# Performance work log

Measured on AMD Instinct MI355X. Metric: run time of the kernel, lower is better.

Reference implementation:

```python
import jax, jax.numpy as jnp
from jax import lax
import numpy as np

B, H, W, C = 8, 32, 32, 256
SOFTMAX_SCALE = 10.0
DN = ('NHWC', 'HWIO', 'NHWC')


def _patches(t):
    # t: [b,h,w,c] -> [b,h,w,3,3,c], SAME zero padding, stride 1 (tf.image.extract_patches)
    b, h, w, c = t.shape
    tp = jnp.pad(t, ((0, 0), (1, 1), (1, 1), (0, 0)))
    cols = [tp[:, i:i + h, j:j + w, :] for i in range(3) for j in range(3)]
    return jnp.stack(cols, axis=3).reshape(b, h, w, 3, 3, c)


def _diag_fuse(z):
    # conv2d of [L,L] map with eye(3) kernel, SAME padding:
    # out[i,j] = z[i-1,j-1] + z[i,j] + z[i+1,j+1] (zero padded)
    dr = jnp.pad(z, ((1, 0), (1, 0)))[:-1, :-1]
    ul = jnp.pad(z, ((0, 1), (0, 1)))[1:, 1:]
    return z + dr + ul


def _conv(x, w):
    return lax.conv_general_dilated(x, w, (1, 1), 'SAME', dimension_numbers=DN)


def _attend(xi, wi, mmean):
    # xi: [h,w,c]; wi: [3,3,c,L] patch kernels; mmean: [L] mean of mask patches
    h, w, c = xi.shape
    L = h * w
    norm = jnp.maximum(jnp.sqrt(jnp.sum(wi * wi, axis=(0, 1, 2))), 1e-4)
    yi = _conv(xi[None], wi / norm)[0]  # [h,w,L] cosine-sim scores
    # fuse: diagonal propagation along both spatial orderings
    z = yi.reshape(L, L)
    z = _diag_fuse(z).reshape(h, w, h, w).transpose(1, 0, 3, 2).reshape(L, L)
    z = _diag_fuse(z).reshape(w, h, w, h).transpose(1, 0, 3, 2)  # [h,w,h,w]
    yi = z.reshape(h, w, L)
    mm = (mmean == 1.0).astype(yi.dtype)  # valid-patch mask per location
    yi = jax.nn.softmax(yi * mm * SOFTMAX_SCALE, axis=-1) * mm
    # conv2d_transpose(yi, wi, stride 1, SAME) == conv with hw-flipped kernel,
    # in/out channels swapped (TF filter layout [h,w,out=C,in=L])
    k2 = jnp.flip(wi, (0, 1)).transpose(0, 1, 3, 2)  # [3,3,L,C]
    return _conv(yi[None], k2)[0]  # [h,w,c]


def _forward(x, mask, conv_w, conv_b, conv1_w, conv1_b, conv2_w, conv2_b):
    b, h, w, c = x.shape
    L = h * w
    # rate=1: tf.image.resize to same size is identity, f == b == x
    wi = _patches(x).reshape(b, L, 3, 3, c).transpose(0, 2, 3, 4, 1)  # [b,3,3,c,L]
    mmean = _patches(mask).mean(axis=(3, 4, 5)).reshape(b, L)
    y = jax.vmap(_attend)(x, wi, mmean)  # [b,h,w,c]
    ycat = jnp.concatenate([y, x], axis=-1)  # [b,h,w,2c]
    g1 = jax.nn.sigmoid(_conv(ycat, conv1_w) + conv1_b)
    g2 = jax.nn.sigmoid(_conv(ycat, conv2_w) + conv2_b)
    gate = (g1 + g2) * 0.5
    out = gate * (_conv(ycat, conv_w) + conv_b)
    return out, jnp.ones_like(mask)


def setup_inputs() -> dict:
    key = jax.random.key(0)
    ks = jax.random.split(key, 4)
    x = jax.random.normal(ks[0], (B, H, W, C), jnp.float32)
    mask = jnp.ones((B, H, W, 1), jnp.float32)
    conv_w = jax.random.normal(ks[1], (3, 3, 2 * C, C), jnp.float32) * 0.02
    conv_b = jnp.zeros((C,), jnp.float32)
    conv1_w = jax.random.normal(ks[2], (1, 1, 2 * C, C), jnp.float32) * 0.02
    conv1_b = jnp.zeros((C,), jnp.float32)
    conv2_w = jax.random.normal(ks[3], (3, 3, 2 * C, C), jnp.float32) * 0.02
    conv2_b = jnp.zeros((C,), jnp.float32)
    return {'x': x, 'mask': mask, 'conv_w': conv_w, 'conv_b': conv_b,
            'conv1_w': conv1_w, 'conv1_b': conv1_b, 'conv2_w': conv2_w, 'conv2_b': conv2_b}


def reference(x, mask, conv_w, conv_b, conv1_w, conv1_b, conv2_w, conv2_b):
    return _forward(x, mask, conv_w, conv_b, conv1_w, conv1_b, conv2_w, conv2_b)
```

## Files before the change

### kernel.cpp

```cpp
#include <hip/hip_runtime.h>
#include <math.h>

typedef unsigned short u16;
typedef __bf16 bf16x8 __attribute__((ext_vector_type(8)));
typedef float f32x4 __attribute__((ext_vector_type(4)));

#define NPOS 1156
#define GSTR 1160
#define GOFF (GSTR * 1156)
#define YSTR 1032
#define YOFF (YSTR * 1026)
#define POS34(p) ((((p) >> 5) + 1) * 34 + ((p) & 31) + 1)

__device__ __constant__ const int kDiagOff[9] = {
    -35 * (GSTR + 1), -34 * (GSTR + 1), -33 * (GSTR + 1),
    -1 * (GSTR + 1),  0,                1 * (GSTR + 1),
    33 * (GSTR + 1),  34 * (GSTR + 1),  35 * (GSTR + 1)};

__device__ __forceinline__ u16 f2bf(float f) {
  unsigned int u = __builtin_bit_cast(unsigned int, f);
  return (u16)((u + 0x7FFFu + ((u >> 16) & 1u)) >> 16);
}
__device__ __forceinline__ float bf2f(u16 v) {
  unsigned int u = ((unsigned int)v) << 16;
  return __builtin_bit_cast(float, u);
}
__device__ __forceinline__ void gload16(const void* g, void* l) {
  __builtin_amdgcn_global_load_lds(
      (const __attribute__((address_space(1))) void*)g,
      (__attribute__((address_space(3))) void*)l, 16, 0, 0);
}
__device__ __forceinline__ int posOf(int p) { return POS34(p); }

__global__ __launch_bounds__(256) void zb_pre(
    float* __restrict__ Gpad, u16* __restrict__ Ylin,
    u16* __restrict__ xpad, u16* __restrict__ ypad) {
  int bi = blockIdx.x, tid = threadIdx.x;
  if (bi < 9248) {
    int b = bi / 1156, r = bi - b * 1156;
    float* row = Gpad + (size_t)b * GOFF + (size_t)r * GSTR;
    int rm = r % 34;
    bool brow = (r < 34) || (r >= 1122) || (rm == 0) || (rm == 33);
    if (brow) {
      for (int c = tid; c < GSTR; c += 256) row[c] = 0.f;
    } else {
      for (int c = tid; c < GSTR; c += 256) {
        int cm = c % 34;
        if (c < 34 || c >= 1122 || cm == 0 || cm == 33) row[c] = 0.f;
      }
    }
    return;
  }
  bi -= 9248;
  if (bi < 8208) {
    int b = bi / 1026, r = bi - b * 1026;
    u16* row = Ylin + (size_t)b * YOFF + (size_t)r * YSTR;
    if (r == 0 || r == 1025) {
      for (int c = tid; c < YSTR; c += 256) row[c] = 0;
    } else if (tid < 8) {
      row[tid == 0 ? 0 : 1024 + tid] = 0;
    }
    return;
  }
  bi -= 8208;
  int arr = bi / 9248;
  bi -= arr * 9248;
  int b = bi / 1156, p = bi - b * 1156;
  int pm = p % 34;
  bool bp = (p < 34) || (p >= 1122) || (pm == 0) || (pm == 33);
  if (!bp) return;
  u16* dst = (arr ? ypad : xpad) + ((size_t)b * NPOS + p) * 256;
  dst[tid] = 0;
}

__global__ __launch_bounds__(256) void zb_apad(u16* __restrict__ Apad2) {
  int bi = blockIdx.x, tid = threadIdx.x;
  int b = bi / 1156, r = bi - b * 1156;
  u16* row = Apad2 + (size_t)b * GOFF + (size_t)r * GSTR;
  int rm = r % 34;
  bool brow = (r < 34) || (r >= 1122) || (rm == 0) || (rm == 33);
  if (brow) {
    for (int c = tid; c < GSTR; c += 256) row[c] = 0;
  } else {
    for (int c = tid; c < GSTR; c += 256) {
      int cm = c % 34;
      if (c < 34 || c >= 1122 || cm == 0 || cm == 33) row[c] = 0;
    }
  }
}

__global__ __launch_bounds__(256) void cast_x(
    const float* __restrict__ x, u16* __restrict__ xpad, u16* __restrict__ xT) {
  int blk = blockIdx.x;
  int b = blk >> 5, h = blk & 31;
  __shared__ u16 T[256][33];
  const float* xrow = x + ((size_t)b * 1024 + h * 32) * 256;
  int tid = threadIdx.x;
  for (int idx = tid; idx < 8192; idx += 256) {
    int w = idx >> 8, c = idx & 255;
    u16 v = f2bf(xrow[(size_t)w * 256 + c]);
    T[c][w] = v;
    xpad[((size_t)b * NPOS + (h + 1) * 34 + (w + 1)) * 256 + c] = v;
  }
  __syncthreads();
  int c = tid;
  unsigned int* dp = (unsigned int*)(xT + ((size_t)(b * 256 + c)) * 1024 + h * 32);
  const unsigned int* sp = (const unsigned int*)&T[c][0];
#pragma unroll
  for (int u = 0; u < 16; ++u) dp[u] = sp[u];
}

__global__ __launch_bounds__(256) void wtrans(
    const float* __restrict__ src, u16* __restrict__ dst, int K) {
  int k0 = blockIdx.x * 32;
  __shared__ u16 T[256][34];
  int tid = threadIdx.x;
  for (int idx = tid; idx < 8192; idx += 256) {
    int kr = idx >> 8, c = idx & 255;
    T[c][kr] = f2bf(src[(size_t)(k0 + kr) * 256 + c]);
  }
  __syncthreads();
  int c = tid;
  unsigned int* dp = (unsigned int*)(dst + (size_t)c * K + k0);
  const unsigned int* sp = (const unsigned int*)&T[c][0];
#pragma unroll
  for (int u = 0; u < 16; ++u) dp[u] = sp[u];
}

__global__ __launch_bounds__(256) void gram_base(
    const u16* __restrict__ xpad, float* __restrict__ Gpad) {
  const int b = blockIdx.z;
  const int m0 = blockIdx.x << 7;
  const int n0 = blockIdx.y << 7;
  const u16* xb = xpad + (size_t)b * NPOS * 256;
  __shared__ __align__(16) u16 As[128 * 64];
  __shared__ __align__(16) u16 Bs[128 * 64];
  const int tid = threadIdx.x;
  const int lane = tid & 63;
  const int wave = tid >> 6;
  const int wm = wave >> 1, wn = wave & 1;
  const int srow = lane >> 3;
  const int cswz = ((lane & 7) ^ srow) << 3;
  int pa[4], pb[4];
#pragma unroll
  for (int i = 0; i < 4; ++i) {
    pa[i] = posOf(m0 + wave * 32 + i * 8 + srow);
    pb[i] = posOf(n0 + wave * 32 + i * 8 + srow);
  }
  int aidx[4][2], bidx[4][2];
#pragma unroll
  for (int f = 0; f < 4; ++f)
#pragma unroll
    for (int ks = 0; ks < 2; ++ks) {
      int ra = wm * 64 + f * 16 + (lane & 15);
      int rb = wn * 64 + f * 16 + (lane & 15);
      int k16 = ks * 4 + (lane >> 4);
      aidx[f][ks] = ra * 64 + ((k16 ^ (ra & 7)) << 3);
      bidx[f][ks] = rb * 64 + ((k16 ^ (rb & 7)) << 3);
    }
  f32x4 acc[4][4] = {};
  for (int c0 = 0; c0 < 256; c0 += 64) {
    __syncthreads();
#pragma unroll
    for (int i = 0; i < 4; ++i) {
      gload16(xb + (size_t)pa[i] * 256 + c0 + cswz, &As[(wave * 32 + i * 8) * 64]);
      gload16(xb + (size_t)pb[i] * 256 + c0 + cswz, &Bs[(wave * 32 + i * 8) * 64]);
    }
    __syncthreads();
#pragma unroll
    for (int ks = 0; ks < 2; ++ks) {
      bf16x8 a[4], bb[4];
#pragma unroll
      for (int f = 0; f < 4; ++f) a[f] = *(const bf16x8*)(As + aidx[f][ks]);
#pragma unroll
      for (int f = 0; f < 4; ++f) bb[f] = *(const bf16x8*)(Bs + bidx[f][ks]);
#pragma unroll
      for (int mi = 0; mi < 4; ++mi)
#pragma unroll
        for (int ni = 0; ni < 4; ++ni)
          acc[mi][ni] = __builtin_amdgcn_mfma_f32_16x16x32_bf16(a[mi], bb[ni], acc[mi][ni], 0, 0, 0);
    }
  }
  float* Gb = Gpad + (size_t)b * GOFF;
  const int r0 = (lane >> 4) << 2;
  const int cb0 = n0 + wn * 64 + (lane & 15);
#pragma unroll
  for (int mi = 0; mi < 4; ++mi) {
    int row = m0 + wm * 64 + mi * 16 + r0;
    int rp = POS34(row);
#pragma unroll
    for (int ni = 0; ni < 4; ++ni) {
      int cp = POS34(cb0 + ni * 16);
#pragma unroll
      for (int r = 0; r < 4; ++r)
        Gb[(size_t)(rp + r) * GSTR + cp] = acc[mi][ni][r];
    }
  }
}

__global__ __launch_bounds__(256) void norm_mm(
    const float* __restrict__ Gpad, const float* __restrict__ mask,
    float* __restrict__ invn, float* __restrict__ mm, float* __restrict__ ones_out) {
  int idx = blockIdx.x * 256 + threadIdx.x;
  int b = idx >> 10, l = idx & 1023;
  const float* Gb = Gpad + (size_t)b * GOFF;
  size_t dbase = (size_t)POS34(l) * (GSTR + 1);
  float d = 0.f;
#pragma unroll
  for (int t = 0; t < 9; ++t) d += Gb[dbase + kDiagOff[t]];
  invn[idx] = 1.0f / fmaxf(sqrtf(d), 1e-4f);
  int lh = l >> 5, lw = l & 31;
  float s = 0.f;
  for (int dh = -1; dh <= 1; ++dh)
    for (int dw = -1; dw <= 1; ++dw) {
      int hh = lh + dh, wv = lw + dw;
      if (hh >= 0 && hh < 32 && wv >= 0 && wv < 32) s += mask[b * 1024 + hh * 32 + wv];
    }
  mm[idx] = ((s / 9.0f) == 1.0f) ? 1.0f : 0.0f;
  ones_out[idx] = 1.0f;
}

__global__ __launch_bounds__(256) void patch_norm_p(
    const float* __restrict__ Gpad, const float* __restrict__ invn,
    u16* __restrict__ Ylin) {
  const int b = blockIdx.y;
  const int p0 = blockIdx.x << 2;
  const float* Gb = Gpad + (size_t)b * GOFF;
  u16* Yb = Ylin + (size_t)b * YOFF;
  const int tid = threadIdx.x;
  const int l0 = tid << 2;
  const int lp0 = POS34(l0);
  const float4 iv = *(const float4*)(invn + (b << 10) + l0);
#pragma unroll
  for (int r = 0; r < 4; ++r) {
    int p = p0 + r;
    int base = POS34(p) * GSTR + lp0;
    float v[9][4];
#pragma unroll
    for (int t = 0; t < 9; ++t) {
      const float* q = Gb + (base + kDiagOff[t]);
      v[t][0] = q[0]; v[t][1] = q[1]; v[t][2] = q[2]; v[t][3] = q[3];
    }
    float s0 = 0.f, s1 = 0.f, s2 = 0.f, s3 = 0.f;
#pragma unroll
    for (int t = 0; t < 9; ++t) { s0 += v[t][0]; s1 += v[t][1]; s2 += v[t][2]; s3 += v[t][3]; }
    u16* yw = Yb + (size_t)(p + 1) * YSTR + l0 + 1;
    yw[0] = f2bf(s0 * iv.x); yw[1] = f2bf(s1 * iv.y);
    yw[2] = f2bf(s2 * iv.z); yw[3] = f2bf(s3 * iv.w);
  }
}

__device__ __forceinline__ float z1p(const u16* __restrict__ Yb, int r, int c) {
  size_t a = (size_t)(r + 1) * YSTR + (c + 1);
  return bf2f(Yb[a]) + bf2f(Yb[a - (YSTR + 1)]) + bf2f(Yb[a + (YSTR + 1)]);
}

__global__ __launch_bounds__(256) void fuse_softmax(
    const u16* __restrict__ Ylin, const float* __restrict__ mm,
    u16* __restrict__ Apad2) {
  const int bi = blockIdx.x;
  const int b = bi >> 10, i = bi & 1023;
  const u16* Yb = Ylin + (size_t)b * YOFF;
  __shared__ float smm[1024];
  __shared__ float red[256];
  const int tid = threadIdx.x;
  for (int t = tid; t < 1024; t += 256) smm[t] = mm[(b << 10) + t];
  __syncthreads();
  const int si = ((i & 31) << 5) | (i >> 5);
  const int rm = (si >= 1) ? ((((si - 1) & 31) << 5) | ((si - 1) >> 5)) : -1;
  const int rp = (si <= 1022) ? ((((si + 1) & 31) << 5) | ((si + 1) >> 5)) : -1;
  float logit[4];
  float lmax = -3.0e38f;
#pragma unroll
  for (int q = 0; q < 4; ++q) {
    int j = tid + (q << 8);
    int sj = ((j & 31) << 5) | (j >> 5);
    float S = z1p(Yb, i, j);
    if (rm >= 0 && sj >= 1) {
      int col = (((sj - 1) & 31) << 5) | ((sj - 1) >> 5);
      S += z1p(Yb, rm, col);
    }
    if (rp >= 0 && sj <= 1022) {
      int col = (((sj + 1) & 31) << 5) | ((sj + 1) >> 5);
      S += z1p(Yb, rp, col);
    }
    float lg = S * smm[j] * 10.0f;
    logit[q] = lg;
    lmax = fmaxf(lmax, lg);
  }
  red[tid] = lmax; __syncthreads();
  for (int off = 128; off > 0; off >>= 1) {
    if (tid < off) red[tid] = fmaxf(red[tid], red[tid + off]);
    __syncthreads();
  }
  float M = red[0];
  __syncthreads();
  float ex[4];
  float lsum = 0.f;
#pragma unroll
  for (int q = 0; q < 4; ++q) { ex[q] = expf(logit[q] - M); lsum += ex[q]; }
  red[tid] = lsum; __syncthreads();
  for (int off = 128; off > 0; off >>= 1) {
    if (tid < off) red[tid] += red[tid + off];
    __syncthreads();
  }
  float inv = 1.0f / red[0];
  u16* Ap = Apad2 + (size_t)b * GOFF + (size_t)POS34(i) * GSTR;
#pragma unroll
  for (int q = 0; q < 4; ++q) {
    int j = tid + (q << 8);
    Ap[POS34(j)] = f2bf(smm[j] * ex[q] * inv);
  }
}

__global__ __launch_bounds__(256) void afuse_p(
    const u16* __restrict__ Apad2, u16* __restrict__ Afuse) {
  const int b = blockIdx.y;
  const int q0 = blockIdx.x << 2;
  const u16* Ab = Apad2 + (size_t)b * GOFF;
  u16* Fb = Afuse + ((size_t)b << 20);
  const int tid = threadIdx.x;
  const int l0 = tid << 2;
  const int lp0 = POS34(l0);
#pragma unroll
  for (int r = 0; r < 4; ++r) {
    int q = q0 + r;
    int base = POS34(q) * GSTR + lp0;
    float v[9][4];
#pragma unroll
    for (int t = 0; t < 9; ++t) {
      const u16* p = Ab + (base - kDiagOff[t]);
      v[t][0] = bf2f(p[0]); v[t][1] = bf2f(p[1]);
      v[t][2] = bf2f(p[2]); v[t][3] = bf2f(p[3]);
    }
    float s0 = 0.f, s1 = 0.f, s2 = 0.f, s3 = 0.f;
#pragma unroll
    for (int t = 0; t < 9; ++t) { s0 += v[t][0]; s1 += v[t][1]; s2 += v[t][2]; s3 += v[t][3]; }
    u16* fw = Fb + (size_t)q * 1024 + l0;
    fw[0] = f2bf(s0); fw[1] = f2bf(s1); fw[2] = f2bf(s2); fw[3] = f2bf(s3);
  }
}

__global__ __launch_bounds__(256) void paste_gemm(
    const u16* __restrict__ Afuse, const u16* __restrict__ xT, u16* __restrict__ ypad) {
  const int bm0 = blockIdx.x << 6;
  const int b = bm0 >> 10;
  const int q0 = bm0 & 1023;
  const int n0 = blockIdx.y << 6;
  const u16* Ab = Afuse + ((size_t)b << 20);
  const u16* xTb = xT + ((size_t)b << 18);
  __shared__ __align__(16) u16 As[64 * 64];
  __shared__ __align__(16) u16 Bs[64 * 64];
  const int tid = threadIdx.x;
  const int lane = tid & 63;
  const int wave = tid >> 6;
  const int wm = wave >> 1, wn = wave & 1;
  const int srow = lane >> 3;
  const int cswz = ((lane & 7) ^ srow) << 3;
  int aidx[2][2], bidx[2][2];
#pragma unroll
  for (int ks = 0; ks < 2; ++ks) {
    int k16 = ks * 4 + (lane >> 4);
#pragma unroll
    for (int f = 0; f < 2; ++f) {
      int ra = wm * 32 + f * 16 + (lane & 15);
      aidx[f][ks] = ra * 64 + ((k16 ^ (ra & 7)) << 3);
      int rb = wn * 32 + f * 16 + (lane & 15);
      bidx[f][ks] = rb * 64 + ((k16 ^ (rb & 7)) << 3);
    }
  }
  f32x4 acc[2][2] = {};
  for (int l0 = 0; l0 < 1024; l0 += 64) {
    __syncthreads();
#pragma unroll
    for (int i = 0; i < 2; ++i) {
      int ar = wave * 16 + i * 8 + srow;
      gload16(Ab + (size_t)(q0 + ar) * 1024 + l0 + cswz, &As[ar * 64]);
      gload16(xTb + (size_t)(n0 + ar) * 1024 + l0 + cswz, &Bs[ar * 64]);
    }
    __syncthreads();
#pragma unroll
    for (int ks = 0; ks < 2; ++ks) {
      bf16x8 a[2], bb[2];
#pragma unroll
      for (int f = 0; f < 2; ++f) a[f] = *(const bf16x8*)(As + aidx[f][ks]);
#pragma unroll
      for (int f = 0; f < 2; ++f) bb[f] = *(const bf16x8*)(Bs + bidx[f][ks]);
#pragma unroll
      for (int mi = 0; mi < 2; ++mi)
#pragma unroll
        for (int ni = 0; ni < 2; ++ni)
          acc[mi][ni] = __builtin_amdgcn_mfma_f32_16x16x32_bf16(a[mi], bb[ni], acc[mi][ni], 0, 0, 0);
    }
  }
  u16* yb = ypad + (size_t)b * NPOS * 256;
  const int r0 = (lane >> 4) << 2;
#pragma unroll
  for (int mi = 0; mi < 2; ++mi) {
    int qb = q0 + wm * 32 + mi * 16 + r0;
#pragma unroll
    for (int ni = 0; ni < 2; ++ni) {
      int c = n0 + wn * 32 + ni * 16 + (lane & 15);
#pragma unroll
      for (int r = 0; r < 4; ++r)
        yb[(size_t)posOf(qb + r) * 256 + c] = f2bf(acc[mi][ni][r]);
    }
  }
}

__global__ __launch_bounds__(256) void conv_split(
    const u16* __restrict__ ypad, const u16* __restrict__ xpad,
    const u16* __restrict__ w0T, const u16* __restrict__ w2T,
    float* __restrict__ c0buf, float* __restrict__ c2buf) {
  const int m0 = blockIdx.x << 6;
  const int b = m0 >> 10;
  const int q0 = m0 & 1023;
  const int sel = blockIdx.y >> 2;
  const int n0 = (blockIdx.y & 3) << 6;
  const u16* wT = sel ? w2T : w0T;
  float* dst = sel ? c2buf : c0buf;
  const u16* yb = ypad + (size_t)b * NPOS * 256;
  const u16* xb = xpad + (size_t)b * NPOS * 256;
  __shared__ __align__(16) u16 As[64 * 64];
  __shared__ __align__(16) u16 Bs[64 * 64];
  const int tid = threadIdx.x;
  const int lane = tid & 63;
  const int wave = tid >> 6;
  const int wm = wave >> 1, wn = wave & 1;
  const int srow = lane >> 3;
  const int cswz = ((lane & 7) ^ srow) << 3;
  int posA[2];
#pragma unroll
  for (int i = 0; i < 2; ++i) posA[i] = posOf(q0 + wave * 16 + i * 8 + srow);
  const u16* wrow[2];
#pragma unroll
  for (int i = 0; i < 2; ++i)
    wrow[i] = wT + (size_t)(n0 + wave * 16 + i * 8 + srow) * 4608 + cswz;
  int aidx[2][2], bidx[2][2];
#pragma unroll
  for (int ks = 0; ks < 2; ++ks) {
    int k16 = ks * 4 + (lane >> 4);
#pragma unroll
    for (int f = 0; f < 2; ++f) {
      int ra = wm * 32 + f * 16 + (lane & 15);
      aidx[f][ks] = ra * 64 + ((k16 ^ (ra & 7)) << 3);
      int rb = wn * 32 + f * 16 + (lane & 15);
      bidx[f][ks] = rb * 64 + ((k16 ^ (rb & 7)) << 3);
    }
  }
  f32x4 acc[2][2] = {};
  for (int kt = 0; kt < 72; ++kt) {
    const int s = kt >> 3;
    const int c0k = (kt & 7) << 6;
    const u16* basep = (c0k < 256) ? yb : xb;
    const int coff = c0k & 255;
    const int dpos = (s / 3 - 1) * 34 + (s % 3 - 1);
    __syncthreads();
#pragma unroll
    for (int i = 0; i < 2; ++i) {
      int ar = wave * 16 + i * 8 + srow;
      gload16(basep + (size_t)(posA[i] + dpos) * 256 + coff + cswz, &As[ar * 64]);
      gload16(wrow[i] + (kt << 6), &Bs[ar * 64]);
    }
    __syncthreads();
#pragma unroll
    for (int ks = 0; ks < 2; ++ks) {
      bf16x8 a[2], bb[2];
#pragma unroll
      for (int f = 0; f < 2; ++f) a[f] = *(const bf16x8*)(As + aidx[f][ks]);
#pragma unroll
      for (int f = 0; f < 2; ++f) bb[f] = *(const bf16x8*)(Bs + bidx[f][ks]);
#pragma unroll
      for (int mi = 0; mi < 2; ++mi)
#pragma unroll
        for (int ni = 0; ni < 2; ++ni)
          acc[mi][ni] = __builtin_amdgcn_mfma_f32_16x16x32_bf16(a[mi], bb[ni], acc[mi][ni], 0, 0, 0);
    }
  }
  const int r0 = (lane >> 4) << 2;
#pragma unroll
  for (int mi = 0; mi < 2; ++mi) {
    int m = m0 + wm * 32 + mi * 16 + r0;
#pragma unroll
    for (int ni = 0; ni < 2; ++ni) {
      int co = n0 + wn * 32 + ni * 16 + (lane & 15);
#pragma unroll
      for (int r = 0; r < 4; ++r)
        dst[(size_t)(m + r) * 256 + co] = acc[mi][ni][r];
    }
  }
}

__global__ __launch_bounds__(256) void conv1_gemm(
    const u16* __restrict__ ypad, const u16* __restrict__ xpad,
    const u16* __restrict__ w1T, float* __restrict__ c1buf) {
  const int m0 = blockIdx.x << 6;
  const int b = m0 >> 10;
  const int q0 = m0 & 1023;
  const int n0 = blockIdx.y << 6;
  const u16* yb = ypad + (size_t)b * NPOS * 256;
  const u16* xb = xpad + (size_t)b * NPOS * 256;
  __shared__ __align__(16) u16 As[64 * 64];
  __shared__ __align__(16) u16 Bs[64 * 64];
  const int tid = threadIdx.x;
  const int lane = tid & 63;
  const int wave = tid >> 6;
  const int wm = wave >> 1, wn = wave & 1;
  const int srow = lane >> 3;
  const int cswz = ((lane & 7) ^ srow) << 3;
  int posA[2];
#pragma unroll
  for (int i = 0; i < 2; ++i) posA[i] = posOf(q0 + wave * 16 + i * 8 + srow);
  int aidx[2][2], bidx[2][2];
#pragma unroll
  for (int ks = 0; ks < 2; ++ks) {
    int k16 = ks * 4 + (lane >> 4);
#pragma unroll
    for (int f = 0; f < 2; ++f) {
      int ra = wm * 32 + f * 16 + (lane & 15);
      aidx[f][ks] = ra * 64 + ((k16 ^ (ra & 7)) << 3);
      int rb = wn * 32 + f * 16 + (lane & 15);
      bidx[f][ks] = rb * 64 + ((k16 ^ (rb & 7)) << 3);
    }
  }
  f32x4 acc[2][2] = {};
  for (int kt = 0; kt < 8; ++kt) {
    const int c0k = kt << 6;
    const u16* basep = (c0k < 256) ? yb : xb;
    const int coff = c0k & 255;
    __syncthreads();
#pragma unroll
    for (int i = 0; i < 2; ++i) {
      int ar = wave * 16 + i * 8 + srow;
      gload16(basep + (size_t)posA[i] * 256 + coff + cswz, &As[ar * 64]);
      gload16(w1T + (size_t)(n0 + ar) * 512 + c0k + cswz, &Bs[ar * 64]);
    }
    __syncthreads();
#pragma unroll
    for (int ks = 0; ks < 2; ++ks) {
      bf16x8 a[2], bb[2];
#pragma unroll
      for (int f = 0; f < 2; ++f) a[f] = *(const bf16x8*)(As + aidx[f][ks]);
#pragma unroll
      for (int f = 0; f < 2; ++f) bb[f] = *(const bf16x8*)(Bs + bidx[f][ks]);
#pragma unroll
      for (int mi = 0; mi < 2; ++mi)
#pragma unroll
        for (int ni = 0; ni < 2; ++ni)
          acc[mi][ni] = __builtin_amdgcn_mfma_f32_16x16x32_bf16(a[mi], bb[ni], acc[mi][ni], 0, 0, 0);
    }
  }
  const int r0 = (lane >> 4) << 2;
#pragma unroll
  for (int mi = 0; mi < 2; ++mi) {
    int m = m0 + wm * 32 + mi * 16 + r0;
#pragma unroll
    for (int ni = 0; ni < 2; ++ni) {
      int co = n0 + wn * 32 + ni * 16 + (lane & 15);
#pragma unroll
      for (int r = 0; r < 4; ++r)
        c1buf[(size_t)(m + r) * 256 + co] = acc[mi][ni][r];
    }
  }
}

__global__ __launch_bounds__(256) void gate_out(
    const float* __restrict__ c0buf, const float* __restrict__ c1buf,
    const float* __restrict__ c2buf, const float* __restrict__ b0,
    const float* __restrict__ b1, const float* __restrict__ b2,
    float* __restrict__ out) {
  size_t i4 = ((size_t)blockIdx.x * 256 + threadIdx.x) * 4;
  int co = (int)(i4 & 255);
  float4 v0 = *(const float4*)(c0buf + i4);
  float4 v1 = *(const float4*)(c1buf + i4);
  float4 v2 = *(const float4*)(c2buf + i4);
  float4 q0 = *(const float4*)(b0 + co);
  float4 q1 = *(const float4*)(b1 + co);
  float4 q2 = *(const float4*)(b2 + co);
  float4 o;
  const float* pv0 = (const float*)&v0; const float* pv1 = (const float*)&v1;
  const float* pv2 = (const float*)&v2; const float* pq0 = (const float*)&q0;
  const float* pq1 = (const float*)&q1; const float* pq2 = (const float*)&q2;
  float* po = (float*)&o;
#pragma unroll
  for (int j = 0; j < 4; ++j) {
    float g1 = 1.f / (1.f + expf(-(pv1[j] + pq1[j])));
    float g2 = 1.f / (1.f + expf(-(pv2[j] + pq2[j])));
    po[j] = 0.5f * (g1 + g2) * (pv0[j] + pq0[j]);
  }
  *(float4*)(out + i4) = o;
}


extern "C" void kernel_launch(void* const* d_in, const int* in_sizes, int n_in,
                              void* d_out, int out_size, void* d_ws, size_t ws_size,
                              hipStream_t stream) {
  const float* x = (const float*)d_in[0];
  const float* mask = (const float*)d_in[1];
  const float* conv_w = (const float*)d_in[2];
  const float* conv_b = (const float*)d_in[3];
  const float* conv1_w = (const float*)d_in[4];
  const float* conv1_b = (const float*)d_in[5];
  const float* conv2_w = (const float*)d_in[6];
  const float* conv2_b = (const float*)d_in[7];
  float* out = (float*)d_out;
  char* wsb = (char*)d_ws;

  float* Gpad  = (float*)(wsb + 0);
  u16* Apad2   = (u16*)(wsb + 0);
  float* c0buf = (float*)(wsb + 0);
  float* c2buf = (float*)(wsb + 8388608);
  float* c1buf = (float*)(wsb + 16777216);
  u16* Ylin    = (u16*)(wsb + 42910720);
  u16* Afuse   = (u16*)(wsb + 42910720);
  u16* xpad    = (u16*)(wsb + 59852032);
  u16* ypad    = (u16*)(wsb + 64587008);
  u16* xT      = (u16*)(wsb + 69321984);
  u16* w0T     = (u16*)(wsb + 73516288);
  u16* w2T     = (u16*)(wsb + 75875584);
  u16* w1T     = (u16*)(wsb + 78234880);
  float* invn  = (float*)(wsb + 78497024);
  float* mmb   = (float*)(wsb + 78529792);

  zb_pre<<<35952, 256, 0, stream>>>(Gpad, Ylin, xpad, ypad);
  cast_x<<<256, 256, 0, stream>>>(x, xpad, xT);
  wtrans<<<144, 256, 0, stream>>>(conv_w, w0T, 4608);
  wtrans<<<144, 256, 0, stream>>>(conv2_w, w2T, 4608);
  wtrans<<<16, 256, 0, stream>>>(conv1_w, w1T, 512);

  gram_base<<<dim3(8, 8, 8), 256, 0, stream>>>(xpad, Gpad);
  norm_mm<<<32, 256, 0, stream>>>(Gpad, mask, invn, mmb, out + 2097152);
  patch_norm_p<<<dim3(256, 8), 256, 0, stream>>>(Gpad, invn, Ylin);
  zb_apad<<<9248, 256, 0, stream>>>(Apad2);
  fuse_softmax<<<8192, 256, 0, stream>>>(Ylin, mmb, Apad2);
  afuse_p<<<dim3(256, 8), 256, 0, stream>>>(Apad2, Afuse);
  paste_gemm<<<dim3(128, 4), 256, 0, stream>>>(Afuse, xT, ypad);
  conv1_gemm<<<dim3(128, 4), 256, 0, stream>>>(ypad, xpad, w1T, c1buf);
  conv_split<<<dim3(128, 8), 256, 0, stream>>>(ypad, xpad, w0T, w2T, c0buf, c2buf);
  gate_out<<<2048, 256, 0, stream>>>(c0buf, c1buf, c2buf, conv_b, conv1_b, conv2_b, out);
}
```

Measured before the change: 281.4 us.

## Band fuse_softmax with LDS row cache and wave reductions; widen conv_split M tile

Each fuse_softmax block now handles four consecutive rows, one wave per row. For interior rows it stages the 18 neighbouring Ylin rows in LDS through async global-to-LDS loads, so the diagonal-fusion gathers hit shared memory instead of global memory. The block-wide shared-memory reductions become wave shuffle reductions, and the mask values are read straight into registers. Separately, conv_split moves from a 64x64 to a 128x64 output tile, which reuses each weight tile across twice as many rows but costs more registers and launches fewer blocks.

```diff
diff --git a/kernel.cpp b/kernel.cpp
--- a/kernel.cpp
+++ b/kernel.cpp
@@ -31,6 +31,17 @@
       (__attribute__((address_space(3))) void*)l, 16, 0, 0);
 }
 __device__ __forceinline__ int posOf(int p) { return POS34(p); }
+
+__device__ __forceinline__ float wredmax(float v) {
+#pragma unroll
+  for (int m = 32; m; m >>= 1) v = fmaxf(v, __shfl_xor(v, m));
+  return v;
+}
+__device__ __forceinline__ float wredsum(float v) {
+#pragma unroll
+  for (int m = 32; m; m >>= 1) v += __shfl_xor(v, m);
+  return v;
+}
 
 __global__ __launch_bounds__(256) void zb_pre(
     float* __restrict__ Gpad, u16* __restrict__ Ylin,
@@ -250,66 +261,94 @@
   }
 }
 
+#define CSTR 1032
+
 __device__ __forceinline__ float z1p(const u16* __restrict__ Yb, int r, int c) {
   size_t a = (size_t)(r + 1) * YSTR + (c + 1);
   return bf2f(Yb[a]) + bf2f(Yb[a - (YSTR + 1)]) + bf2f(Yb[a + (YSTR + 1)]);
 }
 
-__global__ __launch_bounds__(256) void fuse_softmax(
+__global__ __launch_bounds__(256) void fuse_softmax_band(
     const u16* __restrict__ Ylin, const float* __restrict__ mm,
     u16* __restrict__ Apad2) {
   const int bi = blockIdx.x;
-  const int b = bi >> 10, i = bi & 1023;
+  const int b = bi >> 8;
+  const int i0 = (bi & 255) << 2;
   const u16* Yb = Ylin + (size_t)b * YOFF;
-  __shared__ float smm[1024];
-  __shared__ float red[256];
+  const float* mmb = mm + (b << 10);
   const int tid = threadIdx.x;
-  for (int t = tid; t < 1024; t += 256) smm[t] = mm[(b << 10) + t];
-  __syncthreads();
-  const int si = ((i & 31) << 5) | (i >> 5);
-  const int rm = (si >= 1) ? ((((si - 1) & 31) << 5) | ((si - 1) >> 5)) : -1;
-  const int rp = (si <= 1022) ? ((((si + 1) & 31) << 5) | ((si + 1) >> 5)) : -1;
-  float logit[4];
+  const int w = tid >> 6;
+  const int lane = tid & 63;
+  const int i = i0 + w;
+  __shared__ __align__(16) u16 cache[18 * CSTR];
+  const bool interior = (i0 >= 32) && (i0 <= 988);
+  float logit[16];
+  float mmv[16];
   float lmax = -3.0e38f;
-#pragma unroll
-  for (int q = 0; q < 4; ++q) {
-    int j = tid + (q << 8);
-    int sj = ((j & 31) << 5) | (j >> 5);
-    float S = z1p(Yb, i, j);
-    if (rm >= 0 && sj >= 1) {
-      int col = (((sj - 1) & 31) << 5) | ((sj - 1) >> 5);
-      S += z1p(Yb, rm, col);
-    }
-    if (rp >= 0 && sj <= 1022) {
-      int col = (((sj + 1) & 31) << 5) | ((sj + 1) >> 5);
-      S += z1p(Yb, rp, col);
-    }
-    float lg = S * smm[j] * 10.0f;
-    logit[q] = lg;
-    lmax = fmaxf(lmax, lg);
-  }
-  red[tid] = lmax; __syncthreads();
-  for (int off = 128; off > 0; off >>= 1) {
-    if (tid < off) red[tid] = fmaxf(red[tid], red[tid + off]);
-    __syncthreads();
-  }
-  float M = red[0];
-  __syncthreads();
-  float ex[4];
+  if (interior) {
+    for (int ch = tid; ch < 18 * 129; ch += 256) {
+      int k = ch / 129;
+      int c8 = (ch - k * 129) << 3;
+      int g = (k < 6) ? (i0 - 32 + k) : (k < 12) ? (i0 + k - 6) : (i0 + 32 + k - 12);
+      gload16(Yb + (size_t)g * YSTR + c8, cache + ch * 8);
+    }
+    __syncthreads();
+    const u16* cu = cache + w * CSTR;
+    const u16* cc = cache + (w + 6) * CSTR;
+    const u16* cl = cache + (w + 12) * CSTR;
+#define Z1C(base, c) (bf2f((base)[(c)]) + bf2f((base)[CSTR + (c) + 1]) + bf2f((base)[2 * CSTR + (c) + 2]))
+#pragma unroll
+    for (int q = 0; q < 16; ++q) {
+      int j = lane + (q << 6);
+      int sj = ((j & 31) << 5) | (j >> 5);
+      float S = Z1C(cc, j);
+      if (sj >= 1) {
+        int col = (((sj - 1) & 31) << 5) | ((sj - 1) >> 5);
+        S += Z1C(cu, col);
+      }
+      if (sj <= 1022) {
+        int col = (((sj + 1) & 31) << 5) | ((sj + 1) >> 5);
+        S += Z1C(cl, col);
+      }
+      mmv[q] = mmb[j];
+      float lg = S * mmv[q] * 10.0f;
+      logit[q] = lg;
+      lmax = fmaxf(lmax, lg);
+    }
+  } else {
+    const int si = ((i & 31) << 5) | (i >> 5);
+    const int rm = (si >= 1) ? ((((si - 1) & 31) << 5) | ((si - 1) >> 5)) : -1;
+    const int rp = (si <= 1022) ? ((((si + 1) & 31) << 5) | ((si + 1) >> 5)) : -1;
+#pragma unroll
+    for (int q = 0; q < 16; ++q) {
+      int j = lane + (q << 6);
+      int sj = ((j & 31) << 5) | (j >> 5);
+      float S = z1p(Yb, i, j);
+      if (rm >= 0 && sj >= 1) {
+        int col = (((sj - 1) & 31) << 5) | ((sj - 1) >> 5);
+        S += z1p(Yb, rm, col);
+      }
+      if (rp >= 0 && sj <= 1022) {
+        int col = (((sj + 1) & 31) << 5) | ((sj + 1) >> 5);
+        S += z1p(Yb, rp, col);
+      }
+      mmv[q] = mmb[j];
+      float lg = S * mmv[q] * 10.0f;
+      logit[q] = lg;
+      lmax = fmaxf(lmax, lg);
+    }
+  }
+  lmax = wredmax(lmax);
   float lsum = 0.f;
 #pragma unroll
-  for (int q = 0; q < 4; ++q) { ex[q] = expf(logit[q] - M); lsum += ex[q]; }
-  red[tid] = lsum; __syncthreads();
-  for (int off = 128; off > 0; off >>= 1) {
-    if (tid < off) red[tid] += red[tid + off];
-    __syncthreads();
-  }
-  float inv = 1.0f / red[0];
+  for (int q = 0; q < 16; ++q) { logit[q] = expf(logit[q] - lmax); lsum += logit[q]; }
+  lsum = wredsum(lsum);
+  float inv = 1.0f / lsum;
   u16* Ap = Apad2 + (size_t)b * GOFF + (size_t)POS34(i) * GSTR;
 #pragma unroll
-  for (int q = 0; q < 4; ++q) {
-    int j = tid + (q << 8);
-    Ap[POS34(j)] = f2bf(smm[j] * ex[q] * inv);
+  for (int q = 0; q < 16; ++q) {
+    int j = lane + (q << 6);
+    Ap[POS34(j)] = f2bf(mmv[q] * logit[q] * inv);
   }
 }
 
@@ -412,16 +451,16 @@
     const u16* __restrict__ ypad, const u16* __restrict__ xpad,
     const u16* __restrict__ w0T, const u16* __restrict__ w2T,
     float* __restrict__ c0buf, float* __restrict__ c2buf) {
-  const int m0 = blockIdx.x << 6;
+  const int m0 = blockIdx.x << 7;
   const int b = m0 >> 10;
   const int q0 = m0 & 1023;
-  const int sel = blockIdx.y >> 2;
-  const int n0 = (blockIdx.y & 3) << 6;
+  const int sel = blockIdx.z;
+  const int n0 = blockIdx.y << 6;
   const u16* wT = sel ? w2T : w0T;
   float* dst = sel ? c2buf : c0buf;
   const u16* yb = ypad + (size_t)b * NPOS * 256;
   const u16* xb = xpad + (size_t)b * NPOS * 256;
-  __shared__ __align__(16) u16 As[64 * 64];
+  __shared__ __align__(16) u16 As[128 * 64];
   __shared__ __align__(16) u16 Bs[64 * 64];
   const int tid = threadIdx.x;
   const int lane = tid & 63;
@@ -429,26 +468,29 @@
   const int wm = wave >> 1, wn = wave & 1;
   const int srow = lane >> 3;
   const int cswz = ((lane & 7) ^ srow) << 3;
-  int posA[2];
-#pragma unroll
-  for (int i = 0; i < 2; ++i) posA[i] = posOf(q0 + wave * 16 + i * 8 + srow);
+  int posA[4];
+#pragma unroll
+  for (int i = 0; i < 4; ++i) posA[i] = posOf(q0 + wave * 32 + i * 8 + srow);
   const u16* wrow[2];
 #pragma unroll
   for (int i = 0; i < 2; ++i)
     wrow[i] = wT + (size_t)(n0 + wave * 16 + i * 8 + srow) * 4608 + cswz;
-  int aidx[2][2], bidx[2][2];
+  int aidx[4][2], bidx[2][2];
 #pragma unroll
   for (int ks = 0; ks < 2; ++ks) {
     int k16 = ks * 4 + (lane >> 4);
 #pragma unroll
+    for (int f = 0; f < 4; ++f) {
+      int ra = wm * 64 + f * 16 + (lane & 15);
+      aidx[f][ks] = ra * 64 + ((k16 ^ (ra & 7)) << 3);
+    }
+#pragma unroll
     for (int f = 0; f < 2; ++f) {
-      int ra = wm * 32 + f * 16 + (lane & 15);
-      aidx[f][ks] = ra * 64 + ((k16 ^ (ra & 7)) << 3);
       int rb = wn * 32 + f * 16 + (lane & 15);
       bidx[f][ks] = rb * 64 + ((k16 ^ (rb & 7)) << 3);
     }
   }
-  f32x4 acc[2][2] = {};
+  f32x4 acc[4][2] = {};
   for (int kt = 0; kt < 72; ++kt) {
     const int s = kt >> 3;
     const int c0k = (kt & 7) << 6;
@@ -457,21 +499,22 @@
     const int dpos = (s / 3 - 1) * 34 + (s % 3 - 1);
     __syncthreads();
 #pragma unroll
-    for (int i = 0; i < 2; ++i) {
-      int ar = wave * 16 + i * 8 + srow;
-      gload16(basep + (size_t)(posA[i] + dpos) * 256 + coff + cswz, &As[ar * 64]);
-      gload16(wrow[i] + (kt << 6), &Bs[ar * 64]);
-    }
+    for (int i = 0; i < 4; ++i)
+      gload16(basep + (size_t)(posA[i] + dpos) * 256 + coff + cswz,
+              &As[(wave * 32 + i * 8) * 64]);
+#pragma unroll
+    for (int i = 0; i < 2; ++i)
+      gload16(wrow[i] + (kt << 6), &Bs[(wave * 16 + i * 8) * 64]);
     __syncthreads();
 #pragma unroll
     for (int ks = 0; ks < 2; ++ks) {
-      bf16x8 a[2], bb[2];
-#pragma unroll
-      for (int f = 0; f < 2; ++f) a[f] = *(const bf16x8*)(As + aidx[f][ks]);
+      bf16x8 a[4], bb[2];
+#pragma unroll
+      for (int f = 0; f < 4; ++f) a[f] = *(const bf16x8*)(As + aidx[f][ks]);
 #pragma unroll
       for (int f = 0; f < 2; ++f) bb[f] = *(const bf16x8*)(Bs + bidx[f][ks]);
 #pragma unroll
-      for (int mi = 0; mi < 2; ++mi)
+      for (int mi = 0; mi < 4; ++mi)
 #pragma unroll
         for (int ni = 0; ni < 2; ++ni)
           acc[mi][ni] = __builtin_amdgcn_mfma_f32_16x16x32_bf16(a[mi], bb[ni], acc[mi][ni], 0, 0, 0);
@@ -479,8 +522,8 @@
   }
   const int r0 = (lane >> 4) << 2;
 #pragma unroll
-  for (int mi = 0; mi < 2; ++mi) {
-    int m = m0 + wm * 32 + mi * 16 + r0;
+  for (int mi = 0; mi < 4; ++mi) {
+    int m = m0 + wm * 64 + mi * 16 + r0;
 #pragma unroll
     for (int ni = 0; ni < 2; ++ni) {
       int co = n0 + wn * 32 + ni * 16 + (lane & 15);
@@ -632,10 +675,10 @@
   norm_mm<<<32, 256, 0, stream>>>(Gpad, mask, invn, mmb, out + 2097152);
   patch_norm_p<<<dim3(256, 8), 256, 0, stream>>>(Gpad, invn, Ylin);
   zb_apad<<<9248, 256, 0, stream>>>(Apad2);
-  fuse_softmax<<<8192, 256, 0, stream>>>(Ylin, mmb, Apad2);
+  fuse_softmax_band<<<2048, 256, 0, stream>>>(Ylin, mmb, Apad2);
   afuse_p<<<dim3(256, 8), 256, 0, stream>>>(Apad2, Afuse);
   paste_gemm<<<dim3(128, 4), 256, 0, stream>>>(Afuse, xT, ypad);
   conv1_gemm<<<dim3(128, 4), 256, 0, stream>>>(ypad, xpad, w1T, c1buf);
-  conv_split<<<dim3(128, 8), 256, 0, stream>>>(ypad, xpad, w0T, w2T, c0buf, c2buf);
+  conv_split<<<dim3(64, 4, 2), 256, 0, stream>>>(ypad, xpad, w0T, w2T, c0buf, c2buf);
   gate_out<<<2048, 256, 0, stream>>>(c0buf, c1buf, c2buf, conv_b, conv1_b, conv2_b, out);
 }
```

Result: slower. 291.5 us (+3.6%).
